# Performance work log

Hardware: AMD Instinct MI355X
Metric: run time of the kernel (lower is better)

The kernel has to match this reference:

```python
import jax, jax.numpy as jnp
import numpy as np


def setup_inputs() -> dict:
    key = jax.random.key(0)
    ks = jax.random.split(key, 6)
    B, N, D, E = 16, 64, 256, 256
    nodes = jax.random.normal(ks[0], (B * N, D), jnp.float32)
    edges = jax.random.normal(ks[1], (B * N * N, E), jnp.float32)
    W_in = jax.random.normal(ks[2], (2 * D + E, D), jnp.float32) / np.float32(np.sqrt(2 * D + E))
    b_in = jnp.zeros((D,), jnp.float32)
    W_coef = jax.random.normal(ks[3], (D, 1), jnp.float32) / np.float32(np.sqrt(D))
    b_coef = jnp.zeros((1,), jnp.float32)
    W_out = jax.random.normal(ks[4], (D, D), jnp.float32) / np.float32(np.sqrt(D))
    b_out = jnp.zeros((D,), jnp.float32)
    return {"nodes": nodes, "edges": edges, "W_in": W_in, "b_in": b_in,
            "W_coef": W_coef, "b_coef": b_coef, "W_out": W_out, "b_out": b_out,
            "B": B, "N": N}


def reference(nodes, edges, W_in, b_in, W_coef, b_coef, W_out, b_out, B, N):
    # Uniform nums = [N]*B special case of the ragged torch loop.
    D = nodes.shape[-1]
    n3 = nodes.reshape(B, N, D)
    # pair[b,i,j] = [node_i, node_j, edge_ij]  -> [B,N,N,2D+E]
    pair = jnp.concatenate([
        jnp.broadcast_to(n3[:, :, None, :], (B, N, N, D)),
        jnp.broadcast_to(n3[:, None, :, :], (B, N, N, D)),
        edges.reshape(B, N, N, -1),
    ], axis=-1)
    h = jax.nn.relu(pair @ W_in + b_in)            # [B,N,N,D]
    coefs = h @ W_coef + b_coef                    # [B,N,N,1]
    diag = jnp.eye(N, dtype=coefs.dtype)[None, :, :, None] * jnp.float32(1e9)
    attn = jax.nn.softmax(coefs - diag, axis=2)    # softmax over j, diag masked
    residual = jnp.sum(attn * h, axis=2)           # [B,N,D]
    new_nodes = nodes + jax.nn.relu(residual.reshape(B * N, D) @ W_out + b_out)
    return new_nodes, h.reshape(B * N * N, D)
```

## Files before the change

kernel.cpp:

```cpp
#include <hip/hip_runtime.h>
#include <hip/hip_bf16.h>

typedef unsigned int u32;
typedef unsigned short u16;
typedef __attribute__((ext_vector_type(8))) short bf16x8;
typedef __attribute__((ext_vector_type(4))) float f32x4;
typedef __attribute__((ext_vector_type(4))) float f4;

#define DI __device__ __forceinline__

DI u16 f2bfu(float f){
  union{float f; u32 i;} u; u.f = f;
  u32 lsb = (u.i >> 16) & 1u;
  u.i += 0x7fffu + lsb;
  return (u16)(u.i >> 16);
}

union BU { uint4 v; bf16x8 s; };

__global__ __launch_bounds__(256) void k_pack(const float* __restrict__ W_in,
                                              u16* __restrict__ Wp3,
                                              u16* __restrict__ Wp12)
{
  int idx = blockIdx.x * 256 + threadIdx.x;
  int l = idx & 63;
  int g = idx >> 6;
  int lq = l >> 4, lr = l & 15;
  u16 o[8];
  if (g < 128){
    int nt = g >> 3, kk = g & 7;
    int n  = nt * 16 + lr;
    int k0 = 512 + kk * 32 + lq * 8;
#pragma unroll
    for (int tt = 0; tt < 8; tt++) o[tt] = f2bfu(W_in[(size_t)(k0 + tt) * 256 + n]);
    *(uint4*)(Wp3 + (size_t)idx * 8) = *(uint4*)o;
  } else {
    int g2 = g - 128;
    int half = g2 >> 7, rem = g2 & 127;
    int nt = rem >> 3, kk = rem & 7;
    int n  = nt * 16 + lr;
    int k0 = half * 256 + kk * 32 + lq * 8;
#pragma unroll
    for (int tt = 0; tt < 8; tt++) o[tt] = f2bfu(W_in[(size_t)(k0 + tt) * 256 + n]);
    *(uint4*)(Wp12 + (size_t)g2 * 512 + (size_t)l * 8) = *(uint4*)o;
  }
}

__global__ __launch_bounds__(256) void k_pre(
    const float* __restrict__ nodes, const float* __restrict__ b_in,
    const u16* __restrict__ Wp12, float* __restrict__ P1, float* __restrict__ P2)
{
  const int t = threadIdx.x;
  const int w = t >> 6, l = t & 63, lq = l >> 4, lr = l & 15;
  const int bid = blockIdx.x;
  const int rt = bid >> 3, half = (bid >> 2) & 1, cg = bid & 3;

  bf16x8 af[8];
  {
    const float* ap = nodes + (size_t)(rt * 64 + 16 * w + lr) * 256 + lq * 8;
#pragma unroll
    for (int kk = 0; kk < 8; kk++){
      float4 x = *(const float4*)(ap + kk * 32);
      float4 y = *(const float4*)(ap + kk * 32 + 4);
      bf16x8 a;
      a[0]=(short)f2bfu(x.x); a[1]=(short)f2bfu(x.y); a[2]=(short)f2bfu(x.z); a[3]=(short)f2bfu(x.w);
      a[4]=(short)f2bfu(y.x); a[5]=(short)f2bfu(y.y); a[6]=(short)f2bfu(y.z); a[7]=(short)f2bfu(y.w);
      af[kk] = a;
    }
  }
  const uint4* wp = (const uint4*)(Wp12 + (size_t)half * 128 * 512);
  float* P = half ? P2 : P1;
#pragma unroll
  for (int ntl = 0; ntl < 4; ntl++){
    const int nt = cg * 4 + ntl;
    f32x4 acc = {0.f, 0.f, 0.f, 0.f};
#pragma unroll
    for (int kk = 0; kk < 8; kk++){
      BU bu; bu.v = wp[(nt * 8 + kk) * 64 + l];
      acc = __builtin_amdgcn_mfma_f32_16x16x32_bf16(af[kk], bu.s, acc, 0, 0, 0);
    }
    const int col = nt * 16 + lr;
    const float bv = half ? 0.f : b_in[col];
#pragma unroll
    for (int r = 0; r < 4; r++){
      const int row = rt * 64 + 16 * w + 4 * lq + r;
      P[(size_t)row * 256 + col] = acc[r] + bv;
    }
  }
}

__global__ __launch_bounds__(128, 6) void k_h(
    const float* __restrict__ edges, const u16* __restrict__ Wp3,
    const float* __restrict__ W_coef, const float* __restrict__ P1,
    const float* __restrict__ P2, float* __restrict__ out_h,
    float* __restrict__ coefW)
{
  const int t = threadIdx.x;
  const int w = t >> 6, l = t & 63, lq = l >> 4, lr = l & 15;
  const int bid = blockIdx.x;
  const int xcd  = bid & 7;
  const int rest = bid >> 3;
  const int jh   = rest & 1;
  const int bi   = (xcd << 7) | (rest >> 1);
  const int b = bi >> 6;
  const int jq = jh * 2 + w;
  const int j  = jq * 16 + lr;

  bf16x8 af[8];
  {
    const float* ap = edges + (size_t)bi * 16384 + (size_t)j * 256 + lq * 8;
    float4 x[4], y[4];
#pragma unroll
    for (int kk = 0; kk < 4; kk++){
      x[kk] = *(const float4*)(ap + kk * 32);
      y[kk] = *(const float4*)(ap + kk * 32 + 4);
    }
#pragma unroll
    for (int kk = 0; kk < 4; kk++){
      bf16x8 a;
      a[0]=(short)f2bfu(x[kk].x); a[1]=(short)f2bfu(x[kk].y); a[2]=(short)f2bfu(x[kk].z); a[3]=(short)f2bfu(x[kk].w);
      a[4]=(short)f2bfu(y[kk].x); a[5]=(short)f2bfu(y[kk].y); a[6]=(short)f2bfu(y[kk].z); a[7]=(short)f2bfu(y[kk].w);
      af[kk] = a;
    }
#pragma unroll
    for (int kk = 0; kk < 4; kk++){
      x[kk] = *(const float4*)(ap + (kk + 4) * 32);
      y[kk] = *(const float4*)(ap + (kk + 4) * 32 + 4);
    }
#pragma unroll
    for (int kk = 0; kk < 4; kk++){
      bf16x8 a;
      a[0]=(short)f2bfu(x[kk].x); a[1]=(short)f2bfu(x[kk].y); a[2]=(short)f2bfu(x[kk].z); a[3]=(short)f2bfu(x[kk].w);
      a[4]=(short)f2bfu(y[kk].x); a[5]=(short)f2bfu(y[kk].y); a[6]=(short)f2bfu(y[kk].z); a[7]=(short)f2bfu(y[kk].w);
      af[kk + 4] = a;
    }
  }

  const uint4* wp = (const uint4*)Wp3;
  const float* p1p = P1 + (size_t)bi * 256;
  const float* p2p = P2 + ((size_t)b * 64 + j) * 256;
  float* hop = out_h + ((size_t)bi * 64 + j) * 256;
  float cpart = 0.f;

#pragma unroll
  for (int ntc = 0; ntc < 8; ntc++){
#pragma unroll
    for (int nt2 = 0; nt2 < 2; nt2++){
      const int nt = ntc * 2 + nt2;
      f32x4 acc = {0.f, 0.f, 0.f, 0.f};
#pragma unroll
      for (int kk = 0; kk < 8; kk++){
        BU bu; bu.v = wp[(size_t)(nt * 8 + kk) * 64 + l];
        acc = __builtin_amdgcn_mfma_f32_16x16x32_bf16(bu.s, af[kk], acc, 0, 0, 0);
      }
      const int d0 = nt * 16 + 4 * lq;
      f4 p1v = *(const f4*)(p1p + d0);
      f4 p2v = *(const f4*)(p2p + d0);
      f4 wcv = *(const f4*)(W_coef + d0);
      f4 h;
#pragma unroll
      for (int r = 0; r < 4; r++){
        float xx = acc[r] + p1v[r] + p2v[r];
        h[r] = xx > 0.f ? xx : 0.f;
      }
      *(f4*)(hop + d0) = h;
      cpart += h[0]*wcv[0] + h[1]*wcv[1] + h[2]*wcv[2] + h[3]*wcv[3];
    }
  }

  cpart += __shfl_xor(cpart, 16, 64);
  cpart += __shfl_xor(cpart, 32, 64);
  if (lq == 0) coefW[(size_t)bi * 64 + j] = cpart;
}

__global__ __launch_bounds__(256) void k_attn(
    const float* __restrict__ coefW, const float* __restrict__ b_coef,
    const float* __restrict__ h_in, float* __restrict__ RES)
{
  __shared__ float attnS[64];

  const int t = threadIdx.x;
  const int bid = blockIdx.x;
  const int bi = ((bid & 7) << 7) | (127 - (bid >> 3));
  const int i = bi & 63;

  if (t < 64){
    float val = coefW[(size_t)bi * 64 + t] + b_coef[0] - (t == i ? 1e9f : 0.f);
    float m = val;
#pragma unroll
    for (int off = 32; off >= 1; off >>= 1){ float o = __shfl_xor(m, off, 64); m = m > o ? m : o; }
    float e = __expf(val - m);
    float s = e;
#pragma unroll
    for (int off = 32; off >= 1; off >>= 1) s += __shfl_xor(s, off, 64);
    attnS[t] = e / s;
  }
  __syncthreads();

  {
    const float* hb = h_in + (size_t)bi * 16384;
    float res = 0.f;
#pragma unroll 16
    for (int jj = 0; jj < 64; jj++) res += attnS[jj] * hb[(size_t)jj * 256 + t];
    RES[(size_t)bi * 256 + t] = res;
  }
}

__global__ __launch_bounds__(256) void k_out(
    const float* __restrict__ nodes, const float* __restrict__ RES,
    const float* __restrict__ W_out, const float* __restrict__ b_out,
    float* __restrict__ out_nodes)
{
  __shared__ float sR[4][256];
  const int t = threadIdx.x;
  const int r0 = blockIdx.x * 4;
#pragma unroll
  for (int r = 0; r < 4; r++) sR[r][t] = RES[(size_t)(r0 + r) * 256 + t];
  __syncthreads();

  const float bv = b_out[t];
  float a0 = bv, a1 = bv, a2 = bv, a3 = bv;
#pragma unroll 8
  for (int k = 0; k < 256; k++){
    const float wv = W_out[(size_t)k * 256 + t];
    a0 += sR[0][k] * wv;
    a1 += sR[1][k] * wv;
    a2 += sR[2][k] * wv;
    a3 += sR[3][k] * wv;
  }
  out_nodes[(size_t)(r0 + 0) * 256 + t] = nodes[(size_t)(r0 + 0) * 256 + t] + (a0 > 0.f ? a0 : 0.f);
  out_nodes[(size_t)(r0 + 1) * 256 + t] = nodes[(size_t)(r0 + 1) * 256 + t] + (a1 > 0.f ? a1 : 0.f);
  out_nodes[(size_t)(r0 + 2) * 256 + t] = nodes[(size_t)(r0 + 2) * 256 + t] + (a2 > 0.f ? a2 : 0.f);
  out_nodes[(size_t)(r0 + 3) * 256 + t] = nodes[(size_t)(r0 + 3) * 256 + t] + (a3 > 0.f ? a3 : 0.f);
}

extern "C" void kernel_launch(void* const* d_in, const int* in_sizes, int n_in,
                              void* d_out, int out_size, void* d_ws, size_t ws_size,
                              hipStream_t stream)
{
  const float* nodes  = (const float*)d_in[0];
  const float* edges  = (const float*)d_in[1];
  const float* W_in   = (const float*)d_in[2];
  const float* b_in   = (const float*)d_in[3];
  const float* W_coef = (const float*)d_in[4];
  const float* b_coef = (const float*)d_in[5];
  const float* W_out  = (const float*)d_in[6];
  const float* b_out  = (const float*)d_in[7];
  (void)in_sizes; (void)n_in; (void)out_size; (void)ws_size;

  float* P1  = (float*)d_ws;
  float* P2  = P1 + 262144;
  u16*  Wp3  = (u16*)(P2 + 262144);
  u16*  Wp12 = Wp3 + 65536;
  float* coefW = (float*)(Wp12 + 131072);
  float* RES   = coefW + 65536;

  float* out_nodes = (float*)d_out;
  float* out_h = out_nodes + 262144;

  hipLaunchKernelGGL(k_pack, dim3(96),   dim3(256), 0, stream, W_in, Wp3, Wp12);
  hipLaunchKernelGGL(k_pre,  dim3(128),  dim3(256), 0, stream, nodes, b_in, Wp12, P1, P2);
  hipLaunchKernelGGL(k_h,    dim3(2048), dim3(128), 0, stream,
                     edges, Wp3, W_coef, P1, P2, out_h, coefW);
  hipLaunchKernelGGL(k_attn, dim3(1024), dim3(256), 0, stream,
                     coefW, b_coef, out_h, RES);
  hipLaunchKernelGGL(k_out,  dim3(256),  dim3(256), 0, stream,
                     nodes, RES, W_out, b_out, out_nodes);
}
```

Measured before the change: 200.4 us.

## Stage edge-weight tiles in LDS with double buffering and split softmax from reduction

The edge-projection kernel now uses 256-thread blocks covering a full row of 64 j values. Weight tiles are staged into shared memory via global_load_lds with double buffering, so four waves share one copy instead of each reading the weights from global/L2. The attention kernel is split into a standalone softmax kernel and a reduction kernel. The reduction kernel uses float4 loads and a 4-way j-split with a shared-memory combine. This adds an extra launch, barriers every tile, and lower occupancy per block.

```diff
diff --git a/kernel.cpp b/kernel.cpp
--- a/kernel.cpp
+++ b/kernel.cpp
@@ -17,6 +17,12 @@
 }
 
 union BU { uint4 v; bf16x8 s; };
+
+DI void gld16(const void* g, void* l){
+  __builtin_amdgcn_global_load_lds(
+      (const __attribute__((address_space(1))) void*)g,
+      (__attribute__((address_space(3))) void*)l, 16, 0, 0);
+}
 
 __global__ __launch_bounds__(256) void k_pack(const float* __restrict__ W_in,
                                               u16* __restrict__ Wp3,
@@ -89,22 +95,31 @@
   }
 }
 
-__global__ __launch_bounds__(128, 6) void k_h(
+__global__ __launch_bounds__(256, 3) void k_h(
     const float* __restrict__ edges, const u16* __restrict__ Wp3,
     const float* __restrict__ W_coef, const float* __restrict__ P1,
     const float* __restrict__ P2, float* __restrict__ out_h,
     float* __restrict__ coefW)
 {
+  __shared__ uint4 wS[2][1024];
+
   const int t = threadIdx.x;
   const int w = t >> 6, l = t & 63, lq = l >> 4, lr = l & 15;
   const int bid = blockIdx.x;
-  const int xcd  = bid & 7;
-  const int rest = bid >> 3;
-  const int jh   = rest & 1;
-  const int bi   = (xcd << 7) | (rest >> 1);
+  const int bi = ((bid & 7) << 7) | (bid >> 3);
   const int b = bi >> 6;
-  const int jq = jh * 2 + w;
-  const int j  = jq * 16 + lr;
+  const int j = 16 * w + lr;
+
+  const char* wp3b = (const char*)Wp3;
+  auto stage = [&](int bufi, int ntc){
+    const char* src = wp3b + (size_t)ntc * 16384;
+    char* dst = (char*)&wS[bufi][0];
+#pragma unroll
+    for (int c = 0; c < 4; ++c)
+      gld16(src + (w * 4 + c) * 1024 + l * 16, dst + (w * 4 + c) * 1024);
+  };
+
+  stage(0, 0);
 
   bf16x8 af[8];
   {
@@ -136,21 +151,23 @@
     }
   }
 
-  const uint4* wp = (const uint4*)Wp3;
   const float* p1p = P1 + (size_t)bi * 256;
   const float* p2p = P2 + ((size_t)b * 64 + j) * 256;
   float* hop = out_h + ((size_t)bi * 64 + j) * 256;
   float cpart = 0.f;
 
+  __syncthreads();
+  int buf = 0;
 #pragma unroll
   for (int ntc = 0; ntc < 8; ntc++){
+    if (ntc < 7) stage(buf ^ 1, ntc + 1);
 #pragma unroll
     for (int nt2 = 0; nt2 < 2; nt2++){
       const int nt = ntc * 2 + nt2;
       f32x4 acc = {0.f, 0.f, 0.f, 0.f};
 #pragma unroll
       for (int kk = 0; kk < 8; kk++){
-        BU bu; bu.v = wp[(size_t)(nt * 8 + kk) * 64 + l];
+        BU bu; bu.v = wS[buf][(nt2 * 8 + kk) * 64 + l];
         acc = __builtin_amdgcn_mfma_f32_16x16x32_bf16(bu.s, af[kk], acc, 0, 0, 0);
       }
       const int d0 = nt * 16 + 4 * lq;
@@ -166,6 +183,8 @@
       *(f4*)(hop + d0) = h;
       cpart += h[0]*wcv[0] + h[1]*wcv[1] + h[2]*wcv[2] + h[3]*wcv[3];
     }
+    __syncthreads();
+    buf ^= 1;
   }
 
   cpart += __shfl_xor(cpart, 16, 64);
@@ -173,36 +192,53 @@
   if (lq == 0) coefW[(size_t)bi * 64 + j] = cpart;
 }
 
-__global__ __launch_bounds__(256) void k_attn(
+__global__ __launch_bounds__(256) void k_soft(
     const float* __restrict__ coefW, const float* __restrict__ b_coef,
-    const float* __restrict__ h_in, float* __restrict__ RES)
+    float* __restrict__ attnW)
+{
+  const int t = threadIdx.x;
+  const int w = t >> 6, l = t & 63;
+  const int bi = blockIdx.x * 4 + w;
+  const int i = bi & 63;
+  float val = coefW[(size_t)bi * 64 + l] + b_coef[0] - (l == i ? 1e9f : 0.f);
+  float m = val;
+#pragma unroll
+  for (int off = 32; off >= 1; off >>= 1){ float o = __shfl_xor(m, off, 64); m = m > o ? m : o; }
+  float e = __expf(val - m);
+  float s = e;
+#pragma unroll
+  for (int off = 32; off >= 1; off >>= 1) s += __shfl_xor(s, off, 64);
+  attnW[(size_t)bi * 64 + l] = e / s;
+}
+
+__global__ __launch_bounds__(256, 4) void k_res(
+    const float* __restrict__ attnW, const float* __restrict__ h_in,
+    float* __restrict__ RES)
 {
   __shared__ float attnS[64];
-
-  const int t = threadIdx.x;
+  __shared__ f4 resP[3][64];
+
+  const int t = threadIdx.x;
+  const int q = t >> 6, l = t & 63;
   const int bid = blockIdx.x;
-  const int bi = ((bid & 7) << 7) | (127 - (bid >> 3));
-  const int i = bi & 63;
-
-  if (t < 64){
-    float val = coefW[(size_t)bi * 64 + t] + b_coef[0] - (t == i ? 1e9f : 0.f);
-    float m = val;
-#pragma unroll
-    for (int off = 32; off >= 1; off >>= 1){ float o = __shfl_xor(m, off, 64); m = m > o ? m : o; }
-    float e = __expf(val - m);
-    float s = e;
-#pragma unroll
-    for (int off = 32; off >= 1; off >>= 1) s += __shfl_xor(s, off, 64);
-    attnS[t] = e / s;
-  }
+  const int bi = ((bid & 7) << 7) | (bid >> 3);
+
+  if (t < 64) attnS[t] = attnW[(size_t)bi * 64 + t];
   __syncthreads();
 
-  {
-    const float* hb = h_in + (size_t)bi * 16384;
-    float res = 0.f;
-#pragma unroll 16
-    for (int jj = 0; jj < 64; jj++) res += attnS[jj] * hb[(size_t)jj * 256 + t];
-    RES[(size_t)bi * 256 + t] = res;
+  const f4* hb = (const f4*)(h_in + (size_t)bi * 16384) + l;
+  f4 sum = {0.f, 0.f, 0.f, 0.f};
+#pragma unroll
+  for (int jj = 0; jj < 16; jj++){
+    const int j = jj * 4 + q;
+    f4 v = hb[(size_t)j * 64];
+    sum += attnS[j] * v;
+  }
+  if (q) resP[q - 1][l] = sum;
+  __syncthreads();
+  if (q == 0){
+    f4 r = ((sum + resP[0][l]) + resP[1][l]) + resP[2][l];
+    *((f4*)RES + (size_t)bi * 64 + l) = r;
   }
 }
 
@@ -253,17 +289,18 @@
   u16*  Wp3  = (u16*)(P2 + 262144);
   u16*  Wp12 = Wp3 + 65536;
   float* coefW = (float*)(Wp12 + 131072);
-  float* RES   = coefW + 65536;
+  float* attnW = coefW + 65536;
+  float* RES   = attnW + 65536;
 
   float* out_nodes = (float*)d_out;
   float* out_h = out_nodes + 262144;
 
   hipLaunchKernelGGL(k_pack, dim3(96),   dim3(256), 0, stream, W_in, Wp3, Wp12);
   hipLaunchKernelGGL(k_pre,  dim3(128),  dim3(256), 0, stream, nodes, b_in, Wp12, P1, P2);
-  hipLaunchKernelGGL(k_h,    dim3(2048), dim3(128), 0, stream,
+  hipLaunchKernelGGL(k_h,    dim3(1024), dim3(256), 0, stream,
                      edges, Wp3, W_coef, P1, P2, out_h, coefW);
-  hipLaunchKernelGGL(k_attn, dim3(1024), dim3(256), 0, stream,
-                     coefW, b_coef, out_h, RES);
+  hipLaunchKernelGGL(k_soft, dim3(256),  dim3(256), 0, stream, coefW, b_coef, attnW);
+  hipLaunchKernelGGL(k_res,  dim3(1024), dim3(256), 0, stream, attnW, out_h, RES);
   hipLaunchKernelGGL(k_out,  dim3(256),  dim3(256), 0, stream,
                      nodes, RES, W_out, b_out, out_nodes);
 }
```

After: 185.1 us. 7.6% less time.
